# Kernel tuning notes

Measured on AMD Instinct MI355X. Metric: run time of the kernel, lower is better.

Reference implementation:

```python
import jax, jax.numpy as jnp
import numpy as np

N = 100000      # nodes
E = 1000000     # edges (before self loops)
F_IN = 128      # num_features
G = 512         # graphs in batch
NC = 10         # num_classes
EPS_BN = 1e-5
NEG_SLOPE = 0.2


def setup_inputs() -> dict:
    key = jax.random.key(0)
    ks = iter(jax.random.split(key, 40))
    rn = lambda shape, s=0.1: jax.random.normal(next(ks), shape, jnp.float32) * s
    inp = {
        "x": jax.random.normal(next(ks), (N, F_IN), jnp.float32),
        "edge_index": jax.random.randint(next(ks), (2, E), 0, N),
        "batch": jnp.sort(jax.random.randint(next(ks), (N,), 0, G)),
        "W1": rn((F_IN, 128)), "as1": rn((8, 16)), "ad1": rn((8, 16)), "b1": jnp.zeros((128,), jnp.float32),
        "g1": jnp.ones((128,), jnp.float32), "be1": jnp.zeros((128,), jnp.float32),
        "Wl1": rn((128, 16)), "bl1": jnp.zeros((16,), jnp.float32),
        "gl1": jnp.ones((16,), jnp.float32), "bel1": jnp.zeros((16,), jnp.float32),
        "W2": rn((16, 96)), "as2": rn((4, 24)), "ad2": rn((4, 24)), "b2": jnp.zeros((96,), jnp.float32),
        "g2": jnp.ones((96,), jnp.float32), "be2": jnp.zeros((96,), jnp.float32),
        "Wl2": rn((96, 24)), "bl2": jnp.zeros((24,), jnp.float32),
        "gl2": jnp.ones((24,), jnp.float32), "bel2": jnp.zeros((24,), jnp.float32),
        "W3": rn((24, 64)), "as3": rn((2, 32)), "ad3": rn((2, 32)), "b3": jnp.zeros((64,), jnp.float32),
        "g3": jnp.ones((64,), jnp.float32), "be3": jnp.zeros((64,), jnp.float32),
        # final classifier
        "Wo": rn((64, NC)), "bo": jnp.zeros((NC,), jnp.float32),
    }
    return inp


def _bn(h, gamma, beta):
    # training-mode BatchNorm1d: batch statistics, biased variance
    m = jnp.mean(h, axis=0)
    v = jnp.var(h, axis=0)
    return gamma * (h - m) * jax.lax.rsqrt(v + EPS_BN) + beta


def _gat(h_in, src, dst, W, a_src, a_dst, bias, n):
    heads, ch = a_src.shape
    h = (h_in @ W).reshape(n, heads, ch)                     # [N,H,C]
    alpha_s = jnp.sum(h * a_src, axis=-1)                    # [N,H]
    alpha_d = jnp.sum(h * a_dst, axis=-1)                    # [N,H]
    e = jax.nn.leaky_relu(alpha_s[src] + alpha_d[dst], NEG_SLOPE)   # [E,H]
    emax = jax.ops.segment_max(e, dst, num_segments=n)       # segment softmax over target
    e = jnp.exp(e - emax[dst])
    denom = jax.ops.segment_sum(e, dst, num_segments=n)
    alpha = e / (denom[dst] + 1e-16)                         # [E,H]
    msg = h[src] * alpha[:, :, None]                         # [E,H,C]
    out = jax.ops.segment_sum(msg, dst, num_segments=n)      # [N,H,C]
    return out.reshape(n, heads * ch) + bias


def reference(x, edge_index, batch,
              W1, as1, ad1, b1, g1, be1, Wl1, bl1, gl1, bel1,
              W2, as2, ad2, b2, g2, be2, Wl2, bl2, gl2, bel2,
              W3, as3, ad3, b3, g3, be3, Wo, bo):
    n = x.shape[0]
    loop = jnp.arange(n)
    src = jnp.concatenate([edge_index[0], loop])   # add self loops (PyG default)
    dst = jnp.concatenate([edge_index[1], loop])

    h = jax.nn.relu(_bn(_gat(x, src, dst, W1, as1, ad1, b1, n), g1, be1))
    h = jax.nn.relu(_bn(h @ Wl1 + bl1, gl1, bel1))
    h = jax.nn.relu(_bn(_gat(h, src, dst, W2, as2, ad2, b2, n), g2, be2))
    h = jax.nn.relu(_bn(h @ Wl2 + bl2, gl2, bel2))
    h = jax.nn.relu(_bn(_gat(h, src, dst, W3, as3, ad3, b3, n), g3, be3))

    # global mean pool over graphs
    counts = jax.ops.segment_sum(jnp.ones((n,), h.dtype), batch, num_segments=G)
    pooled = jax.ops.segment_sum(h, batch, num_segments=G) / jnp.maximum(counts, 1.0)[:, None]
    # dropout is identity in eval
    return pooled @ Wo + bo
```

## Files before the change

kernel.cpp:

```cpp
#include <hip/hip_runtime.h>

typedef unsigned short u16;
typedef unsigned int   u32;
typedef unsigned long long u64;
typedef __attribute__((ext_vector_type(8))) short short8;
typedef __attribute__((ext_vector_type(4))) float f32x4;

#define DEVI __device__ __forceinline__

#define NPB 256
#define SHB 8
#define BHB 64
#define PST 256
#define LOG2E 1.44269504088896340736f

DEVI float bf2f(u16 u){ union{u32 i; float f;} x; x.i = ((u32)u)<<16; return x.f; }
DEVI u16 f2bf(float f){ union{float f; u32 i;} x; x.f = f;
  u32 r = (x.i + 0x7FFFu + ((x.i>>16)&1u))>>16; return (u16)r; }
DEVI float lrelu(float x){ return x > 0.f ? x : 0.2f*x; }
DEVI float exp2g(float x){ return __builtin_amdgcn_exp2f(x); }
DEVI float gload(const void* p, size_t i, int f32){
  return f32 ? ((const float*)p)[i] : bf2f(((const u16*)p)[i]);
}

__global__ __launch_bounds__(256) void k_prep(const void* x, const void* W1,
    const void* W2, const void* as2, const void* ad2,
    const void* W3, const void* as3, const void* ad3,
    int* dflag, u16* Wt, u16* Wbd2, u16* Wbd3, float* prepF, int* cnts)
{
  __shared__ int sf32;
  if (threadIdx.x == 0){
    const u16* p = (const u16*)x;
    int hits = 0;
    for (int j = 0; j < 512; j++){
      u16 e = (p[j] >> 7) & 0xFF;
      if (e >= 0xC0) hits++;
    }
    sf32 = hits ? 1 : 0;
    if (blockIdx.x == 0) *dflag = sf32;
  }
  __syncthreads();
  const int f32 = sf32;
  int b = blockIdx.x, t = threadIdx.x;
  if (b < 16){
    for (int i = b*256 + t; i < 128*128; i += 16*256){
      int k = i >> 7, nn = i & 127;
      Wt[nn*128 + k] = f2bf(gload(W1, i, f32));
    }
  } else if (b == 16){
    for (int i = t; i < 64*96; i += 256){
      int r = i/96, m = i - r*96;
      int h = r >> 4, k = r & 15;
      float v = ((m/24) == h) ? gload(W2, k*96 + m, f32) : 0.f;
      Wbd2[i] = f2bf(v);
    }
    if (t < 64){
      int h = t >> 4, k = t & 15;
      float s = 0.f, d = 0.f;
      for (int c = 0; c < 24; c++){
        float w = gload(W2, k*96 + h*24 + c, f32);
        s = fmaf(w, gload(as2, h*24 + c, f32), s);
        d = fmaf(w, gload(ad2, h*24 + c, f32), d);
      }
      prepF[t] = s; prepF[64 + t] = d;
    }
  } else {
    for (int i = t; i < 48*64; i += 256){
      int r = i >> 6, m = i & 63;
      int h = r/24, k = r - h*24;
      float v = ((m >> 5) == h) ? gload(W3, k*64 + m, f32) : 0.f;
      Wbd3[i] = f2bf(v);
    }
    if (t < 48){
      int h = t/24, k = t - h*24;
      float s = 0.f, d = 0.f;
      for (int c = 0; c < 32; c++){
        float w = gload(W3, k*64 + h*32 + c, f32);
        s = fmaf(w, gload(as3, h*32 + c, f32), s);
        d = fmaf(w, gload(ad3, h*32 + c, f32), d);
      }
      prepF[128 + t] = s; prepF[176 + t] = d;
    }
    if (t >= 64 && t < 72) cnts[t - 64] = 0;
  }
}

__global__ __launch_bounds__(1024) void k_bhist(const int* ei, int E, int* hist, int NB){
  __shared__ int lh[512];
  for (int b = threadIdx.x; b < NB; b += 1024) lh[b] = 0;
  __syncthreads();
  for (int e = blockIdx.x*1024 + threadIdx.x; e < E; e += BHB*1024)
    atomicAdd(&lh[((u32)ei[E + e]) >> SHB], 1);
  __syncthreads();
  for (int b = threadIdx.x; b < NB; b += 1024) hist[blockIdx.x*NB + b] = lh[b];
}

__global__ __launch_bounds__(512) void k_bmid(int* hist, int* base, int* coff, int NB, int N){
  __shared__ int l[512];
  int t = threadIdx.x;
  int s = 0;
  if (t < NB){
    #pragma unroll 8
    for (int j = 0; j < BHB; j++) s += hist[j*NB + t];
  }
  l[t] = s; __syncthreads();
  for (int st = 1; st < 512; st <<= 1){
    int a = (t >= st) ? l[t - st] : 0;
    __syncthreads();
    l[t] += a;
    __syncthreads();
  }
  int run0 = l[t] - s;
  if (t < NB){
    base[t] = run0;
    int run = run0;
    for (int j = 0; j < BHB; j++){
      int v = hist[j*NB + t];
      hist[j*NB + t] = run;
      run += v;
    }
  }
  if (t == 511){ base[NB] = l[511]; coff[N] = l[511]; }
}

__global__ __launch_bounds__(1024) void k_bfill(const int* ei, int E, const int* hist,
                                                u64* tmp, int NB){
  __shared__ int cur[512];
  for (int b = threadIdx.x; b < NB; b += 1024) cur[b] = hist[blockIdx.x*NB + b];
  __syncthreads();
  for (int e = blockIdx.x*1024 + threadIdx.x; e < E; e += BHB*1024){
    int s = ei[e], d = ei[E + e];
    int p = atomicAdd(&cur[((u32)d) >> SHB], 1);
    tmp[p] = ((u64)(u32)d << 32) | (u32)s;
  }
}

__global__ __launch_bounds__(256) void k_cfill(const u64* tmp, const int* base,
                                               int* coff, int* csr, int N){
  __shared__ int cnt[NPB], start[NPB];
  int b = blockIdx.x, t = threadIdx.x;
  int p0 = base[b], p1 = base[b + 1];
  cnt[t] = 0;
  __syncthreads();
  for (int i = p0 + t; i < p1; i += 256)
    atomicAdd(&cnt[(int)(tmp[i] >> 32) & (NPB - 1)], 1);
  __syncthreads();
  if (t == 0){
    int run = p0;
    for (int j = 0; j < NPB; j++){ start[j] = run; run += cnt[j]; }
  }
  __syncthreads();
  {
    int node = b*NPB + t;
    if (node < N) coff[node] = start[t];
    cnt[t] = 0;
  }
  __syncthreads();
  for (int i = p0 + t; i < p1; i += 256){
    u64 pr = tmp[i];
    int dj = (int)(pr >> 32) & (NPB - 1);
    int r = atomicAdd(&cnt[dj], 1);
    csr[start[dj] + r] = (int)(u32)pr;
  }
}

__global__ __launch_bounds__(256) void k_mfma1A(const void* x, const u16* __restrict__ Wt,
    const void* a_s, const void* a_d,
    u16* __restrict__ out, u16* __restrict__ als, u16* __restrict__ ald,
    int n, const int* dflag)
{
  const int f32 = dflag[0];
  const int wave = threadIdx.x >> 6;
  const int lane = threadIdx.x & 63;
  const int l15 = lane & 15, q = lane >> 4;
  const int arow = blockIdx.x*64 + wave*16 + l15;
  const bool rok = arow < n;

  f32x4 acc[8];
  #pragma unroll
  for (int t = 0; t < 8; t++) acc[t] = {0.f, 0.f, 0.f, 0.f};

  #pragma unroll
  for (int kk = 0; kk < 4; kk++){
    short8 a = {0,0,0,0,0,0,0,0};
    if (rok){
      const int ko = kk*32 + q*8;
      if (f32){
        const float* xp = (const float*)x + (size_t)arow*128 + ko;
        float4 v0 = *(const float4*)xp;
        float4 v1 = *(const float4*)(xp + 4);
        a[0]=(short)f2bf(v0.x); a[1]=(short)f2bf(v0.y); a[2]=(short)f2bf(v0.z); a[3]=(short)f2bf(v0.w);
        a[4]=(short)f2bf(v1.x); a[5]=(short)f2bf(v1.y); a[6]=(short)f2bf(v1.z); a[7]=(short)f2bf(v1.w);
      } else {
        a = *(const short8*)((const u16*)x + (size_t)arow*128 + ko);
      }
    }
    #pragma unroll
    for (int t = 0; t < 8; t++){
      short8 b = *(const short8*)(Wt + (size_t)(l15 + 16*t)*128 + kk*32 + q*8);
      acc[t] = __builtin_amdgcn_mfma_f32_16x16x32_bf16(a, b, acc[t], 0, 0, 0);
    }
  }

  const int orow0 = blockIdx.x*64 + wave*16 + q*4;
  #pragma unroll
  for (int r = 0; r < 4; r++){
    int orow = orow0 + r;
    if (orow < n){
      #pragma unroll
      for (int t = 0; t < 8; t++)
        out[(size_t)orow*128 + l15 + 16*t] = f2bf(acc[t][r]);
    }
  }

  float as_l[8], ad_l[8];
  #pragma unroll
  for (int t = 0; t < 8; t++){
    as_l[t] = gload(a_s, t*16 + l15, f32);
    ad_l[t] = gload(a_d, t*16 + l15, f32);
  }
  #pragma unroll
  for (int r = 0; r < 4; r++){
    float s[8], d[8];
    #pragma unroll
    for (int t = 0; t < 8; t++){
      s[t] = acc[t][r] * as_l[t];
      d[t] = acc[t][r] * ad_l[t];
    }
    #pragma unroll
    for (int st = 1; st < 16; st <<= 1){
      #pragma unroll
      for (int t = 0; t < 8; t++){
        s[t] += __shfl_xor(s[t], st);
        d[t] += __shfl_xor(d[t], st);
      }
    }
    int orow = orow0 + r;
    if (l15 == 0 && orow < n){
      short8 sv, dv;
      #pragma unroll
      for (int t = 0; t < 8; t++){
        sv[t] = (short)f2bf(s[t] * LOG2E);
        dv[t] = (short)f2bf(d[t] * LOG2E);
      }
      *(short8*)(als + (size_t)orow*8) = sv;
      *(short8*)(ald + (size_t)orow*8) = dv;
    }
  }
}

template<int K,int M,int RT,int TPB,bool AFFINE,bool WBF16>
__global__ __launch_bounds__(TPB) void k_gemm(
    const u16* in, const void* Wg,
    const float* stat, const void* gam, const void* bet, float invn,
    u16* out, int n, const int* dflag)
{
  constexpr int CT = 4;
  constexpr int TC = M/CT;
  constexpr int TR = TPB/TC;
  constexpr int ROWS = TR*RT;
  static_assert(TPB % TC == 0, "");
  __shared__ __align__(16) u16 Wl[K*M];
  __shared__ float Il[ROWS*(K+1)];
  __shared__ float faL[AFFINE ? K : 1], fdL[AFFINE ? K : 1];

  const int f32 = dflag[0];
  if constexpr (AFFINE){
    for (int k = threadIdx.x; k < K; k += TPB){
      float m = stat[k]*invn;
      float vv = stat[128 + k]*invn - m*m;
      float a = gload(gam, k, f32) * rsqrtf(vv + 1e-5f);
      faL[k] = a;
      fdL[k] = gload(bet, k, f32) - m*a;
    }
    __syncthreads();
  }

  for (int i = threadIdx.x; i < K*M; i += TPB){
    if constexpr (WBF16) Wl[i] = ((const u16*)Wg)[i];
    else Wl[i] = f32 ? f2bf(((const float*)Wg)[i]) : ((const u16*)Wg)[i];
  }

  const int rowbase = blockIdx.x * ROWS;
  for (int i = threadIdx.x; i < ROWS*K; i += TPB){
    int rr = i / K, k = i - rr*K;
    int r = rowbase + rr;
    float v = 0.f;
    if (r < n){
      v = bf2f(in[(size_t)r*K + k]);
      if constexpr (AFFINE) v = fmaxf(fmaf(faL[k], v, fdL[k]), 0.f);
    }
    Il[rr*(K+1) + k] = v;
  }
  __syncthreads();

  const int tc = threadIdx.x % TC;
  const int tr = threadIdx.x / TC;
  float acc[RT][CT];
  #pragma unroll
  for (int j = 0; j < RT; j++)
    #pragma unroll
    for (int c = 0; c < CT; c++) acc[j][c] = 0.f;

  #pragma unroll 8
  for (int k = 0; k < K; k++){
    ushort4 u = *(const ushort4*)&Wl[k*M + tc*CT];
    float w0 = bf2f(u.x), w1 = bf2f(u.y), w2 = bf2f(u.z), w3 = bf2f(u.w);
    #pragma unroll
    for (int j = 0; j < RT; j++){
      float iv = Il[(tr + j*TR)*(K+1) + k];
      acc[j][0] = fmaf(iv, w0, acc[j][0]);
      acc[j][1] = fmaf(iv, w1, acc[j][1]);
      acc[j][2] = fmaf(iv, w2, acc[j][2]);
      acc[j][3] = fmaf(iv, w3, acc[j][3]);
    }
  }

  #pragma unroll
  for (int j = 0; j < RT; j++){
    int r = rowbase + tr + j*TR;
    if (r < n){
      ushort4 st;
      st.x = f2bf(acc[j][0]); st.y = f2bf(acc[j][1]);
      st.z = f2bf(acc[j][2]); st.w = f2bf(acc[j][3]);
      *(ushort4*)&out[(size_t)r*M + tc*CT] = st;
    }
  }
}

template<int H,int C>
__global__ __launch_bounds__(256) void k_pullW(const u16* __restrict__ h,
    const u16* __restrict__ als, const u16* __restrict__ ald,
    const int* __restrict__ off, const int* __restrict__ csr, u16* __restrict__ out, int n)
{
  constexpr int F = H*C;
  constexpr int L = F/2;
  constexpr int LOGH = (H==8)?3:((H==4)?2:1);
  constexpr int EPG = 64 >> LOGH;
  int wid = blockIdx.x*4 + (threadIdx.x >> 6);
  if (wid >= n) return;
  int lane = threadIdx.x & 63;
  int uu = lane >> LOGH;
  int hh = lane & (H-1);
  int fl = (lane < L) ? lane : (L-1);
  int hd = (2*fl)/C;
  const u32* hw = (const u32*)h;

  float adw = bf2f(ald[(u32)wid*H + hh]);
  float wsw = exp2g(lrelu(bf2f(als[(u32)wid*H + hh]) + adw));
  float den_lane = (uu == 0) ? wsw : 0.f;

  float wsf = exp2g(lrelu(bf2f(als[(u32)wid*H + hd]) + bf2f(ald[(u32)wid*H + hd])));
  u32 vs = hw[(u32)wid*L + fl];
  float acc0 = wsf * bf2f((u16)vs);
  float acc1 = wsf * bf2f((u16)(vs >> 16));

  int e0 = off[wid], e1 = off[wid + 1];
  for (int e = e0; e < e1; e += EPG){
    int rem = e1 - e;
    int su = csr[e + (uu < rem ? uu : 0)];
    float w = exp2g(lrelu(bf2f(als[(u32)su*H + hh]) + adw));
    if (uu >= rem) w = 0.f;
    den_lane += w;
    int cnt = rem < EPG ? rem : EPG;
    for (int jj = 0; jj < cnt; jj += 8){
      int sb[8]; float wb[8]; u32 vv[8];
      #pragma unroll
      for (int j = 0; j < 8; j++){
        int sl = ((jj + j) << LOGH) + hd;
        sb[j] = __shfl(su, sl);
        wb[j] = __shfl(w,  sl);
      }
      #pragma unroll
      for (int j = 0; j < 8; j++) vv[j] = hw[(u32)sb[j]*L + fl];
      #pragma unroll
      for (int j = 0; j < 8; j++){
        acc0 = fmaf(wb[j], bf2f((u16)vv[j]), acc0);
        acc1 = fmaf(wb[j], bf2f((u16)(vv[j] >> 16)), acc1);
      }
    }
  }
  #pragma unroll
  for (int st = H; st < 64; st <<= 1) den_lane += __shfl_xor(den_lane, st);
  float den = __shfl(den_lane, hd);
  float r = 1.f/(den + 1e-16f);
  if (lane < L)
    ((u32*)out)[(u32)wid*L + fl] = (u32)f2bf(acc0*r) | ((u32)f2bf(acc1*r) << 16);
}

template<int H,int CIN>
__global__ __launch_bounds__(256) void k_alphaX(const u16* __restrict__ Cb,
    const float* stat, const void* gam, const void* bet, float invn,
    const float* vs, const float* vd,
    u16* act, u16* als, u16* ald, int n, const int* dflag)
{
  const int f32 = dflag[0];
  __shared__ float faL[CIN], fdL[CIN];
  if (threadIdx.x < CIN){
    int k = threadIdx.x;
    float m = stat[k]*invn;
    float vv = stat[128 + k]*invn - m*m;
    float a = gload(gam, k, f32) * rsqrtf(vv + 1e-5f);
    faL[k] = a;
    fdL[k] = gload(bet, k, f32) - m*a;
  }
  __syncthreads();
  int idx = blockIdx.x*256 + threadIdx.x;
  if (idx >= n*H) return;
  int j = idx / H, h = idx - j*H;
  float s = 0.f, d = 0.f;
  #pragma unroll
  for (int k = 0; k < CIN; k++){
    float v = bf2f(Cb[(size_t)j*CIN + k]);
    v = fmaxf(fmaf(faL[k], v, fdL[k]), 0.f);
    s = fmaf(v, vs[h*CIN + k], s);
    d = fmaf(v, vd[h*CIN + k], d);
    if (h == 0) act[(size_t)j*CIN + k] = f2bf(v);
  }
  als[idx] = f2bf(s * LOG2E); ald[idx] = f2bf(d * LOG2E);
}

template<int H,int CIN>
__global__ __launch_bounds__(256) void k_pullX(const u16* __restrict__ act,
    const u16* __restrict__ als, const u16* __restrict__ ald,
    const int* __restrict__ off, const int* __restrict__ csr, u16* __restrict__ D, int n)
{
  constexpr int LX = H*CIN;
  constexpr int LOGH = (H==4)?2:1;
  constexpr int EPG = 64 >> LOGH;
  int wid = blockIdx.x*4 + (threadIdx.x >> 6);
  if (wid >= n) return;
  int lane = threadIdx.x & 63;
  int uu = lane >> LOGH;
  int hh = lane & (H-1);
  int fl = (lane < LX) ? lane : (LX-1);
  int hf = fl / CIN, k = fl - hf*CIN;

  float adw = bf2f(ald[(u32)wid*H + hh]);
  float wsw = exp2g(lrelu(bf2f(als[(u32)wid*H + hh]) + adw));
  float den_lane = (uu == 0) ? wsw : 0.f;

  float wsf = exp2g(lrelu(bf2f(als[(u32)wid*H + hf]) + bf2f(ald[(u32)wid*H + hf])));
  float acc = wsf * bf2f(act[(u32)wid*CIN + k]);

  int e0 = off[wid], e1 = off[wid + 1];
  for (int e = e0; e < e1; e += EPG){
    int rem = e1 - e;
    int su = csr[e + (uu < rem ? uu : 0)];
    float w = exp2g(lrelu(bf2f(als[(u32)su*H + hh]) + adw));
    if (uu >= rem) w = 0.f;
    den_lane += w;
    int cnt = rem < EPG ? rem : EPG;
    for (int jj = 0; jj < cnt; jj += 8){
      int sb[8]; float wb[8]; u16 vv[8];
      #pragma unroll
      for (int j = 0; j < 8; j++){
        int sl = ((jj + j) << LOGH) + hf;
        sb[j] = __shfl(su, sl);
        wb[j] = __shfl(w,  sl);
      }
      #pragma unroll
      for (int j = 0; j < 8; j++) vv[j] = act[(u32)sb[j]*CIN + k];
      #pragma unroll
      for (int j = 0; j < 8; j++) acc = fmaf(wb[j], bf2f(vv[j]), acc);
    }
  }
  #pragma unroll
  for (int st = H; st < 64; st <<= 1) den_lane += __shfl_xor(den_lane, st);
  float den = __shfl(den_lane, hf);
  if (lane < LX)
    D[(u32)wid*LX + fl] = f2bf(acc / (den + 1e-16f));
}

template<int F,int TPB>
__global__ __launch_bounds__(TPB) void k_statAB(const u16* __restrict__ x, int n,
    float* __restrict__ part, float* __restrict__ outS, int* __restrict__ cnt)
{
  constexpr int L = F/2;
  constexpr int RPB = TPB/L;
  static_assert(TPB % L == 0, "");
  int c = threadIdx.x % L;
  int tr = threadIdx.x / L;
  const u32* xw = (const u32*)x;
  int chunk = (n + (int)gridDim.x - 1)/(int)gridDim.x;
  int r0 = blockIdx.x*chunk;
  int r1 = r0 + chunk; if (r1 > n) r1 = n;
  float a0=0.f, a1=0.f, b0=0.f, b1=0.f;
  int r = r0 + tr;
  for (; r + 3*RPB < r1; r += 4*RPB){
    u32 v0 = xw[(size_t)r*L + c];
    u32 v1 = xw[(size_t)(r + RPB)*L + c];
    u32 v2 = xw[(size_t)(r + 2*RPB)*L + c];
    u32 v3 = xw[(size_t)(r + 3*RPB)*L + c];
    float f0 = bf2f((u16)v0), f1 = bf2f((u16)(v0 >> 16));
    float f2 = bf2f((u16)v1), f3 = bf2f((u16)(v1 >> 16));
    float f4 = bf2f((u16)v2), f5 = bf2f((u16)(v2 >> 16));
    float f6 = bf2f((u16)v3), f7 = bf2f((u16)(v3 >> 16));
    a0 += (f0 + f2) + (f4 + f6);
    a1 += (f1 + f3) + (f5 + f7);
    b0 += (f0*f0 + f2*f2) + (f4*f4 + f6*f6);
    b1 += (f1*f1 + f3*f3) + (f5*f5 + f7*f7);
  }
  for (; r < r1; r += RPB){
    u32 v = xw[(size_t)r*L + c];
    float f0 = bf2f((u16)v), f1 = bf2f((u16)(v >> 16));
    a0 += f0; b0 = fmaf(f0, f0, b0);
    a1 += f1; b1 = fmaf(f1, f1, b1);
  }
  __shared__ float l0[TPB], l1[TPB], l2[TPB], l3[TPB];
  l0[threadIdx.x] = a0; l1[threadIdx.x] = a1;
  l2[threadIdx.x] = b0; l3[threadIdx.x] = b1;
  __syncthreads();
  for (int t2 = threadIdx.x; t2 < 256; t2 += TPB){
    int col = t2 & 127;
    float s = 0.f;
    if (col < F){
      int cc = col >> 1, par = col & 1;
      const float* base = (t2 >= 128) ? (par ? l3 : l2) : (par ? l1 : l0);
      #pragma unroll 4
      for (int j = 0; j < RPB; j++) s += base[j*L + cc];
    }
    part[(size_t)blockIdx.x*256 + t2] = s;
  }
  __threadfence();
  __shared__ int lastf;
  if (threadIdx.x == 0) lastf = (atomicAdd(cnt, 1) == (int)gridDim.x - 1) ? 1 : 0;
  __syncthreads();
  if (lastf){
    __threadfence();
    for (int t2 = threadIdx.x; t2 < 256; t2 += TPB){
      float s = 0.f;
      int b = 0;
      for (; b + 3 < PST; b += 4)
        s += (part[(size_t)b*256 + t2] + part[(size_t)(b+1)*256 + t2])
           + (part[(size_t)(b+2)*256 + t2] + part[(size_t)(b+3)*256 + t2]);
      for (; b < PST; b++) s += part[(size_t)b*256 + t2];
      outS[t2] = s;
    }
  }
}

__global__ __launch_bounds__(256) void k_pool(const u16* B, const int* batch, int n,
    const float* stat, const void* g3, const void* be3, float invn,
    const void* Wo, const void* bo, void* outp, const int* dflag)
{
  const int f32 = dflag[0];
  __shared__ float fa[64], fd[64];
  if (threadIdx.x < 64){
    int k = threadIdx.x;
    float m = stat[k]*invn;
    float v = stat[128 + k]*invn - m*m;
    float a = gload(g3, k, f32) * rsqrtf(v + 1e-5f);
    fa[k] = a;
    fd[k] = gload(be3, k, f32) - m*a;
  }
  __syncthreads();

  int g = blockIdx.x;
  int lane = threadIdx.x & 63, wv = threadIdx.x >> 6;
  int s, e;
  { int l = 0, h = n; while (l < h){ int m = (l+h)>>1; if (batch[m] <  g) l = m+1; else h = m; } s = l; }
  { int l = s, h = n; while (l < h){ int m = (l+h)>>1; if (batch[m] <= g) l = m+1; else h = m; } e = l; }
  float a = fa[lane], d = fd[lane], acc = 0.f;
  for (int r = s + wv; r < e; r += 4)
    acc += fmaxf(fmaf(a, bf2f(B[(size_t)r*64 + lane]), d), 0.f);
  __shared__ float pl[4][64];
  pl[wv][lane] = acc;
  __syncthreads();
  if (wv == 0){
    float cnt = (e > s) ? (float)(e - s) : 1.f;
    pl[0][lane] = (pl[0][lane] + pl[1][lane] + pl[2][lane] + pl[3][lane]) / cnt;
  }
  __syncthreads();
  if (threadIdx.x < 10){
    int lo = threadIdx.x;
    float o = gload(bo, lo, f32);
    for (int l2 = 0; l2 < 64; l2++) o = fmaf(pl[0][l2], gload(Wo, l2*10 + lo, f32), o);
    if (f32) ((float*)outp)[g*10 + lo] = o;
    else     ((u16*) outp)[g*10 + lo] = f2bf(o);
  }
}

extern "C" void kernel_launch(void* const* d_in, const int* in_sizes, int n_in,
                              void* d_out, int out_size, void* d_ws, size_t ws_size,
                              hipStream_t stream)
{
  const void* x   = d_in[0];
  const int* ei   = (const int*)d_in[1];
  const int* batch= (const int*)d_in[2];
  const void* W1  = d_in[3];
  const void* as1 = d_in[4];
  const void* ad1 = d_in[5];
  const void* g1  = d_in[7];
  const void* be1 = d_in[8];
  const void* Wl1 = d_in[9];
  const void* gl1 = d_in[11];
  const void* bel1= d_in[12];
  const void* W2  = d_in[13];
  const void* as2 = d_in[14];
  const void* ad2 = d_in[15];
  const void* g2  = d_in[17];
  const void* be2 = d_in[18];
  const void* Wl2 = d_in[19];
  const void* gl2 = d_in[21];
  const void* bel2= d_in[22];
  const void* W3  = d_in[23];
  const void* as3 = d_in[24];
  const void* ad3 = d_in[25];
  const void* g3  = d_in[27];
  const void* be3 = d_in[28];
  const void* Wo  = d_in[29];
  const void* bo  = d_in[30];
  (void)n_in; (void)ws_size;

  const int N = in_sizes[2];
  const int E = in_sizes[1] / 2;
  const int G = out_size / 10;
  const int NB = (N + NPB - 1) >> SHB;

  char* w = (char*)d_ws;
  size_t off = 0;
  auto alloc = [&](size_t bytes)->void*{
    size_t o = off; off += (bytes + 255) & ~(size_t)255; return (void*)(w + o);
  };
  int*   dflag= (int*)alloc(4);
  int*   cnts = (int*)alloc(8*4);
  int*   coff = (int*)alloc((size_t)(N+1)*4);
  int*   csr  = (int*)alloc((size_t)E*4);
  int*   bbase= (int*)alloc((size_t)(NB+1)*4);
  int*   hist = (int*)alloc((size_t)BHB*NB*4);
  float* stS  = (float*)alloc(1280*4);
  float* part = (float*)alloc((size_t)PST*256*4);
  float* prepF= (float*)alloc(256*4);
  u16*   Wt   = (u16*)alloc(128*128*2);
  u16*   Wbd2 = (u16*)alloc(64*96*2);
  u16*   Wbd3 = (u16*)alloc(48*64*2);
  u16*   als  = (u16*)alloc((size_t)N*8*2);
  u16*   ald  = (u16*)alloc((size_t)N*8*2);
  u16*   Cb   = (u16*)alloc((size_t)N*24*2);
  u16*   A    = (u16*)alloc((size_t)N*128*2);
  u16*   B    = (u16*)alloc((size_t)N*128*2);
  u64*   tmp  = (u64*)A;
  u16*   D    = A;
  u16*   act  = A + (size_t)N*64;

  const float invN = 1.f/(float)N;

  k_prep<<<18, 256, 0, stream>>>(x, W1, W2, as2, ad2, W3, as3, ad3,
                                 dflag, Wt, Wbd2, Wbd3, prepF, cnts);

  k_bhist<<<BHB, 1024, 0, stream>>>(ei, E, hist, NB);
  k_bmid <<<1, 512, 0, stream>>>(hist, bbase, coff, NB, N);
  k_bfill<<<BHB, 1024, 0, stream>>>(ei, E, hist, tmp, NB);
  k_cfill<<<NB, 256, 0, stream>>>(tmp, bbase, coff, csr, N);

  k_mfma1A<<<(N+63)/64, 256, 0, stream>>>(x, Wt, as1, ad1, A, als, ald, N, dflag);
  k_pullW<8,16><<<(N+3)/4, 256, 0, stream>>>(A, als, ald, coff, csr, B, N);
  k_statAB<128,256><<<PST, 256, 0, stream>>>(B, N, part, stS + 0, cnts + 0);

  k_gemm<128,16,1,256,true,false><<<(N+63)/64, 256, 0, stream>>>(
      B, Wl1, stS + 0, g1, be1, invN, Cb, N, dflag);
  k_statAB<16,256><<<PST, 256, 0, stream>>>(Cb, N, part, stS + 256, cnts + 1);

  k_alphaX<4,16><<<(N*4+255)/256, 256, 0, stream>>>(
      Cb, stS + 256, gl1, bel1, invN, prepF + 0, prepF + 64, act, als, ald, N, dflag);
  k_pullX<4,16><<<(N+3)/4, 256, 0, stream>>>(act, als, ald, coff, csr, D, N);
  k_gemm<64,96,2,192,false,true><<<(N+15)/16, 192, 0, stream>>>(
      D, Wbd2, nullptr, nullptr, nullptr, invN, B, N, dflag);
  k_statAB<96,192><<<PST, 192, 0, stream>>>(B, N, part, stS + 512, cnts + 2);

  k_gemm<96,24,2,192,true,false><<<(N+63)/64, 192, 0, stream>>>(
      B, Wl2, stS + 512, g2, be2, invN, Cb, N, dflag);
  k_statAB<24,192><<<PST, 192, 0, stream>>>(Cb, N, part, stS + 768, cnts + 3);

  k_alphaX<2,24><<<(N*2+255)/256, 256, 0, stream>>>(
      Cb, stS + 768, gl2, bel2, invN, prepF + 128, prepF + 176, act, als, ald, N, dflag);
  k_pullX<2,24><<<(N+3)/4, 256, 0, stream>>>(act, als, ald, coff, csr, D, N);
  k_gemm<48,64,2,256,false,true><<<(N+31)/32, 256, 0, stream>>>(
      D, Wbd3, nullptr, nullptr, nullptr, invN, B, N, dflag);
  k_statAB<64,256><<<PST, 256, 0, stream>>>(B, N, part, stS + 1024, cnts + 4);

  k_pool<<<G, 256, 0, stream>>>(B, batch, N, stS + 1024, g3, be3, invN, Wo, bo, d_out, dflag);
}
```

Baseline: 716.5 us.

## Parallelize bucket prefix scan across waves, pack CSR temp entries into 32 bits

The single-block bucket scan, which walked 64 histogram rows serially for each bucket, is split into three kernels: a wave-reduction totals kernel, a small scan over bucket totals, and a wave-level exclusive scan that writes per-block cursors. The temporary edge buffer for the CSR build now stores the local destination (8 bits) and the source (24 bits) in a u32 instead of a u64, which halves that traffic. k_alphaX also reads and writes bf16 pairs as 32-bit words. The packing assumes node ids fit in 24 bits, and the scan path adds two kernel launches.

```diff
diff --git a/kernel.cpp b/kernel.cpp
--- a/kernel.cpp
+++ b/kernel.cpp
@@ -95,47 +95,58 @@
   for (int b = threadIdx.x; b < NB; b += 1024) hist[blockIdx.x*NB + b] = lh[b];
 }
 
-__global__ __launch_bounds__(512) void k_bmid(int* hist, int* base, int* coff, int NB, int N){
+__global__ __launch_bounds__(256) void k_btotW(const int* hist, int* tot, int NB){
+  int wv = threadIdx.x >> 6, lane = threadIdx.x & 63;
+  int b = blockIdx.x*4 + wv;
+  if (b >= NB) return;
+  int v = hist[lane*NB + b];
+  #pragma unroll
+  for (int st = 1; st < 64; st <<= 1) v += __shfl_xor(v, st);
+  if (lane == 0) tot[b] = v;
+}
+
+__global__ __launch_bounds__(512) void k_bscan(const int* tot, int* base, int* coff, int NB, int N){
   __shared__ int l[512];
   int t = threadIdx.x;
-  int s = 0;
-  if (t < NB){
-    #pragma unroll 8
-    for (int j = 0; j < BHB; j++) s += hist[j*NB + t];
-  }
-  l[t] = s; __syncthreads();
+  int v = (t < NB) ? tot[t] : 0;
+  l[t] = v; __syncthreads();
   for (int st = 1; st < 512; st <<= 1){
     int a = (t >= st) ? l[t - st] : 0;
     __syncthreads();
     l[t] += a;
     __syncthreads();
   }
-  int run0 = l[t] - s;
-  if (t < NB){
-    base[t] = run0;
-    int run = run0;
-    for (int j = 0; j < BHB; j++){
-      int v = hist[j*NB + t];
-      hist[j*NB + t] = run;
-      run += v;
-    }
-  }
+  if (t < NB) base[t] = l[t] - v;
   if (t == 511){ base[NB] = l[511]; coff[N] = l[511]; }
 }
 
+__global__ __launch_bounds__(256) void k_bcurW(int* hist, const int* base, int NB){
+  int wv = threadIdx.x >> 6, lane = threadIdx.x & 63;
+  int b = blockIdx.x*4 + wv;
+  if (b >= NB) return;
+  int v = hist[lane*NB + b];
+  int sc = v;
+  #pragma unroll
+  for (int d = 1; d < 64; d <<= 1){
+    int t2 = __shfl_up(sc, d);
+    if (lane >= d) sc += t2;
+  }
+  hist[lane*NB + b] = base[b] + sc - v;
+}
+
 __global__ __launch_bounds__(1024) void k_bfill(const int* ei, int E, const int* hist,
-                                                u64* tmp, int NB){
+                                                u32* tmp, int NB){
   __shared__ int cur[512];
   for (int b = threadIdx.x; b < NB; b += 1024) cur[b] = hist[blockIdx.x*NB + b];
   __syncthreads();
   for (int e = blockIdx.x*1024 + threadIdx.x; e < E; e += BHB*1024){
     int s = ei[e], d = ei[E + e];
     int p = atomicAdd(&cur[((u32)d) >> SHB], 1);
-    tmp[p] = ((u64)(u32)d << 32) | (u32)s;
-  }
-}
-
-__global__ __launch_bounds__(256) void k_cfill(const u64* tmp, const int* base,
+    tmp[p] = ((u32)(d & (NPB-1)) << 24) | (u32)s;
+  }
+}
+
+__global__ __launch_bounds__(256) void k_cfill(const u32* tmp, const int* base,
                                                int* coff, int* csr, int N){
   __shared__ int cnt[NPB], start[NPB];
   int b = blockIdx.x, t = threadIdx.x;
@@ -143,7 +154,7 @@
   cnt[t] = 0;
   __syncthreads();
   for (int i = p0 + t; i < p1; i += 256)
-    atomicAdd(&cnt[(int)(tmp[i] >> 32) & (NPB - 1)], 1);
+    atomicAdd(&cnt[tmp[i] >> 24], 1);
   __syncthreads();
   if (t == 0){
     int run = p0;
@@ -157,10 +168,10 @@
   }
   __syncthreads();
   for (int i = p0 + t; i < p1; i += 256){
-    u64 pr = tmp[i];
-    int dj = (int)(pr >> 32) & (NPB - 1);
+    u32 pr = tmp[i];
+    int dj = pr >> 24;
     int r = atomicAdd(&cnt[dj], 1);
-    csr[start[dj] + r] = (int)(u32)pr;
+    csr[start[dj] + r] = (int)(pr & 0xFFFFFFu);
   }
 }
 
@@ -394,6 +405,7 @@
     const float* vs, const float* vd,
     u16* act, u16* als, u16* ald, int n, const int* dflag)
 {
+  constexpr int L2 = CIN/2;
   const int f32 = dflag[0];
   __shared__ float faL[CIN], fdL[CIN];
   if (threadIdx.x < CIN){
@@ -408,14 +420,17 @@
   int idx = blockIdx.x*256 + threadIdx.x;
   if (idx >= n*H) return;
   int j = idx / H, h = idx - j*H;
+  const u32* row32 = (const u32*)Cb + (size_t)j*L2;
+  u32* act32 = (u32*)act + (size_t)j*L2;
   float s = 0.f, d = 0.f;
   #pragma unroll
-  for (int k = 0; k < CIN; k++){
-    float v = bf2f(Cb[(size_t)j*CIN + k]);
-    v = fmaxf(fmaf(faL[k], v, fdL[k]), 0.f);
-    s = fmaf(v, vs[h*CIN + k], s);
-    d = fmaf(v, vd[h*CIN + k], d);
-    if (h == 0) act[(size_t)j*CIN + k] = f2bf(v);
+  for (int k2 = 0; k2 < L2; k2++){
+    u32 v = row32[k2];
+    float v0 = fmaxf(fmaf(faL[2*k2],     bf2f((u16)v),         fdL[2*k2]),     0.f);
+    float v1 = fmaxf(fmaf(faL[2*k2 + 1], bf2f((u16)(v >> 16)), fdL[2*k2 + 1]), 0.f);
+    s = fmaf(v0, vs[h*CIN + 2*k2], s); s = fmaf(v1, vs[h*CIN + 2*k2 + 1], s);
+    d = fmaf(v0, vd[h*CIN + 2*k2], d); d = fmaf(v1, vd[h*CIN + 2*k2 + 1], d);
+    if (h == 0) act32[k2] = (u32)f2bf(v0) | ((u32)f2bf(v1) << 16);
   }
   als[idx] = f2bf(s * LOG2E); ald[idx] = f2bf(d * LOG2E);
 }
@@ -628,6 +643,7 @@
   int*   coff = (int*)alloc((size_t)(N+1)*4);
   int*   csr  = (int*)alloc((size_t)E*4);
   int*   bbase= (int*)alloc((size_t)(NB+1)*4);
+  int*   btot = (int*)alloc((size_t)NB*4);
   int*   hist = (int*)alloc((size_t)BHB*NB*4);
   float* stS  = (float*)alloc(1280*4);
   float* part = (float*)alloc((size_t)PST*256*4);
@@ -640,17 +656,20 @@
   u16*   Cb   = (u16*)alloc((size_t)N*24*2);
   u16*   A    = (u16*)alloc((size_t)N*128*2);
   u16*   B    = (u16*)alloc((size_t)N*128*2);
-  u64*   tmp  = (u64*)A;
+  u32*   tmp  = (u32*)A;
   u16*   D    = A;
   u16*   act  = A + (size_t)N*64;
 
   const float invN = 1.f/(float)N;
+  const int nbw = (NB + 3)/4;
 
   k_prep<<<18, 256, 0, stream>>>(x, W1, W2, as2, ad2, W3, as3, ad3,
                                  dflag, Wt, Wbd2, Wbd3, prepF, cnts);
 
   k_bhist<<<BHB, 1024, 0, stream>>>(ei, E, hist, NB);
-  k_bmid <<<1, 512, 0, stream>>>(hist, bbase, coff, NB, N);
+  k_btotW<<<nbw, 256, 0, stream>>>(hist, btot, NB);
+  k_bscan<<<1, 512, 0, stream>>>(btot, bbase, coff, NB, N);
+  k_bcurW<<<nbw, 256, 0, stream>>>(hist, bbase, NB);
   k_bfill<<<BHB, 1024, 0, stream>>>(ei, E, hist, tmp, NB);
   k_cfill<<<NB, 256, 0, stream>>>(tmp, bbase, coff, csr, N);
 
```

Result: faster. 698.0 us, median of 2 (-2.6%).
